# Kernel tuning notes

Hardware: AMD Instinct MI355X
Metric: run time of the kernel (lower is better)

## Reference

```python
import jax, jax.numpy as jnp
import numpy as np

DIM = 512
HEADS = 8
EPS = 1e-5


def layer_norm(x, g, b):
    mu = jnp.mean(x, axis=-1, keepdims=True)
    var = jnp.mean(jnp.square(x - mu), axis=-1, keepdims=True)
    return (x - mu) * jax.lax.rsqrt(var + EPS) * g + b


def setup_inputs() -> dict:
    key = jax.random.key(0)
    ks = jax.random.split(key, 8)
    d = DIM
    s = 0.02
    return {
        "x": jax.random.normal(ks[0], (2, d, 64, 64), jnp.float32),
        "ln1_g": jnp.ones((d,), jnp.float32),
        "ln1_b": jnp.zeros((d,), jnp.float32),
        "w_qkv": jax.random.normal(ks[1], (d, 3 * d), jnp.float32) * s,
        "b_qkv": jnp.zeros((3 * d,), jnp.float32),
        "w_proj": jax.random.normal(ks[2], (d, d), jnp.float32) * s,
        "b_proj": jnp.zeros((d,), jnp.float32),
        "ln2_g": jnp.ones((d,), jnp.float32),
        "ln2_b": jnp.zeros((d,), jnp.float32),
        "w_ffn1": jax.random.normal(ks[3], (d, 4 * d), jnp.float32) * s,
        "b_ffn1": jnp.zeros((4 * d,), jnp.float32),
        "w_ffn2": jax.random.normal(ks[4], (4 * d, d), jnp.float32) * s,
        "b_ffn2": jnp.zeros((d,), jnp.float32),
    }


def reference(x, ln1_g, ln1_b, w_qkv, b_qkv, w_proj, b_proj,
              ln2_g, ln2_b, w_ffn1, b_ffn1, w_ffn2, b_ffn2):
    B, C, H, W = x.shape
    hd = C // HEADS
    x_in = x
    t = x.reshape(B, C, H * W).transpose(0, 2, 1)  # [B, N, C]
    h = layer_norm(t, ln1_g, ln1_b)
    qkv = h @ w_qkv + b_qkv  # [B, N, 3C]
    q, k, v = jnp.split(qkv, 3, axis=-1)
    def to_heads(a):
        return a.reshape(B, -1, HEADS, hd).transpose(0, 2, 1, 3)  # [B, h, N, hd]
    q, k, v = to_heads(q), to_heads(k), to_heads(v)
    # NOTE: module scales by 1/sqrt(C), not 1/sqrt(head_dim)
    attn = jnp.einsum('bhqd,bhkd->bhqk', q, k) / jnp.sqrt(jnp.float32(C))
    attn = jax.nn.softmax(attn, axis=-1)
    out = jnp.einsum('bhqk,bhkd->bhqd', attn, v)
    out = out.transpose(0, 2, 1, 3).reshape(B, -1, C)
    out = out @ w_proj + b_proj
    t = t + out
    h2 = layer_norm(t, ln2_g, ln2_b)
    ffn = jax.nn.relu(h2 @ w_ffn1 + b_ffn1) @ w_ffn2 + b_ffn2
    t = t + ffn
    y = t.transpose(0, 2, 1).reshape(B, C, H, W)
    return y + x_in
```

## Files before the change

### kernel.cpp

```cpp
#include <hip/hip_runtime.h>
#include <hip/hip_bf16.h>

typedef __bf16 bf16;
typedef __bf16 bf16x8 __attribute__((ext_vector_type(8)));
typedef __bf16 bf16x4 __attribute__((ext_vector_type(4)));
typedef float f32x4 __attribute__((ext_vector_type(4)));
typedef int int4v __attribute__((ext_vector_type(4)));
typedef int int2v __attribute__((ext_vector_type(2)));

#define DEV static __device__ __forceinline__

DEV void gload16(const void* g, void* l) {
    __builtin_amdgcn_global_load_lds(
        (const __attribute__((address_space(1))) void*)g,
        (__attribute__((address_space(3))) void*)l, 16, 0, 0);
}

DEV f32x4 mfma16(bf16x8 a, bf16x8 b, f32x4 c) {
    return __builtin_amdgcn_mfma_f32_16x16x32_bf16(a, b, c, 0, 0, 0);
}

DEV int cvtpk(float lo, float hi) {
    int r;
    asm("v_cvt_pk_bf16_f32 %0, %1, %2" : "=v"(r) : "v"(lo), "v"(hi));
    return r;
}

DEV float rexp2(float x) {
    float r;
    asm("v_exp_f32 %0, %1" : "=v"(r) : "v"(x));
    return r;
}

__global__ __launch_bounds__(256)
void k_transpose_x(const float* __restrict__ x, float* __restrict__ t) {
    __shared__ float tile[32][33];
    int bid = blockIdx.x;
    int nt = bid & 127, ct = (bid >> 7) & 15, b = bid >> 11;
    int n0 = nt * 32, c0 = ct * 32;
    int tid = threadIdx.x;
    const float* xb = x + (size_t)b * 512 * 4096;
    int nl = tid & 31, cl = tid >> 5;
#pragma unroll
    for (int i = 0; i < 4; i++) {
        int c = cl + i * 8;
        tile[c][nl] = xb[(size_t)(c0 + c) * 4096 + n0 + nl];
    }
    __syncthreads();
    float* tb = t + (size_t)b * 4096 * 512;
    int cl2 = tid & 31, nl2 = tid >> 5;
#pragma unroll
    for (int i = 0; i < 4; i++) {
        int n = nl2 + i * 8;
        tb[(size_t)(n0 + n) * 512 + c0 + cl2] = tile[cl2][n];
    }
}

__global__ __launch_bounds__(256)
void k_out3(const float* __restrict__ t, const bf16* __restrict__ f2o,
            const float* __restrict__ x, float* __restrict__ y) {
    __shared__ float tile[32][33];
    int bid = blockIdx.x;
    int nt = bid & 127, ct = (bid >> 7) & 15, b = bid >> 11;
    int n0 = nt * 32, c0 = ct * 32;
    int tid = threadIdx.x;
#pragma unroll
    for (int i = 0; i < 4; i++) {
        int nl = (tid >> 5) + i * 8;
        size_t idx = (size_t)(b * 4096 + n0 + nl) * 512 + c0 + (tid & 31);
        tile[tid & 31][nl] = t[idx] + (float)f2o[idx];
    }
    __syncthreads();
    const float* xb = x + ((size_t)b * 512 + c0) * 4096;
    float* yb = y + ((size_t)b * 512 + c0) * 4096;
#pragma unroll
    for (int i = 0; i < 4; i++) {
        int cl = (tid >> 5) + i * 8;
        int nl = tid & 31;
        size_t off = (size_t)cl * 4096 + n0 + nl;
        yb[off] = tile[cl][nl] + xb[off];
    }
}

__global__ __launch_bounds__(256)
void k_ln(const float* __restrict__ t, const float* __restrict__ gg,
          const float* __restrict__ bb, bf16* __restrict__ h) {
    int lane = threadIdx.x & 63;
    int row = blockIdx.x * 4 + (threadIdx.x >> 6);
    const float* tr = t + (size_t)row * 512;
    f32x4 v0 = *(const f32x4*)(tr + lane * 4);
    f32x4 v1 = *(const f32x4*)(tr + 256 + lane * 4);
    float s = v0[0] + v0[1] + v0[2] + v0[3] + v1[0] + v1[1] + v1[2] + v1[3];
#pragma unroll
    for (int m = 1; m < 64; m <<= 1) s += __shfl_xor(s, m);
    float mu = s * (1.0f / 512.0f);
    float vs = 0.f;
#pragma unroll
    for (int j = 0; j < 4; j++) {
        float d0 = v0[j] - mu, d1 = v1[j] - mu;
        vs += d0 * d0 + d1 * d1;
    }
#pragma unroll
    for (int m = 1; m < 64; m <<= 1) vs += __shfl_xor(vs, m);
    float rs = rsqrtf(vs * (1.0f / 512.0f) + 1e-5f);
    f32x4 g0 = *(const f32x4*)(gg + lane * 4);
    f32x4 g1 = *(const f32x4*)(gg + 256 + lane * 4);
    f32x4 b0 = *(const f32x4*)(bb + lane * 4);
    f32x4 b1 = *(const f32x4*)(bb + 256 + lane * 4);
    bf16x4 o0, o1;
#pragma unroll
    for (int j = 0; j < 4; j++) {
        o0[j] = (bf16)((v0[j] - mu) * rs * g0[j] + b0[j]);
        o1[j] = (bf16)((v1[j] - mu) * rs * g1[j] + b1[j]);
    }
    *(bf16x4*)(h + (size_t)row * 512 + lane * 4) = o0;
    *(bf16x4*)(h + (size_t)row * 512 + 256 + lane * 4) = o1;
}

__global__ __launch_bounds__(256)
void k_lnr(float* __restrict__ t, const bf16* __restrict__ r,
           const float* __restrict__ gg, const float* __restrict__ bb,
           bf16* __restrict__ h) {
    int lane = threadIdx.x & 63;
    int row = blockIdx.x * 4 + (threadIdx.x >> 6);
    float* tr = t + (size_t)row * 512;
    f32x4 v0 = *(const f32x4*)(tr + lane * 4);
    f32x4 v1 = *(const f32x4*)(tr + 256 + lane * 4);
    bf16x4 r0 = *(const bf16x4*)(r + (size_t)row * 512 + lane * 4);
    bf16x4 r1 = *(const bf16x4*)(r + (size_t)row * 512 + 256 + lane * 4);
#pragma unroll
    for (int j = 0; j < 4; j++) {
        v0[j] += (float)r0[j];
        v1[j] += (float)r1[j];
    }
    *(f32x4*)(tr + lane * 4) = v0;
    *(f32x4*)(tr + 256 + lane * 4) = v1;
    float s = v0[0] + v0[1] + v0[2] + v0[3] + v1[0] + v1[1] + v1[2] + v1[3];
#pragma unroll
    for (int m = 1; m < 64; m <<= 1) s += __shfl_xor(s, m);
    float mu = s * (1.0f / 512.0f);
    float vs = 0.f;
#pragma unroll
    for (int j = 0; j < 4; j++) {
        float d0 = v0[j] - mu, d1 = v1[j] - mu;
        vs += d0 * d0 + d1 * d1;
    }
#pragma unroll
    for (int m = 1; m < 64; m <<= 1) vs += __shfl_xor(vs, m);
    float rs = rsqrtf(vs * (1.0f / 512.0f) + 1e-5f);
    f32x4 g0 = *(const f32x4*)(gg + lane * 4);
    f32x4 g1 = *(const f32x4*)(gg + 256 + lane * 4);
    f32x4 b0 = *(const f32x4*)(bb + lane * 4);
    f32x4 b1 = *(const f32x4*)(bb + 256 + lane * 4);
    bf16x4 o0, o1;
#pragma unroll
    for (int j = 0; j < 4; j++) {
        o0[j] = (bf16)((v0[j] - mu) * rs * g0[j] + b0[j]);
        o1[j] = (bf16)((v1[j] - mu) * rs * g1[j] + b1[j]);
    }
    *(bf16x4*)(h + (size_t)row * 512 + lane * 4) = o0;
    *(bf16x4*)(h + (size_t)row * 512 + 256 + lane * 4) = o1;
}

__global__ __launch_bounds__(256)
void k_wt(const float* __restrict__ w, bf16* __restrict__ wt, int K, int N) {
    __shared__ float tile[32][33];
    int ntn = N >> 5;
    int kt = blockIdx.x / ntn, ntile = blockIdx.x % ntn;
    int k0 = kt * 32, n0 = ntile * 32;
    int tid = threadIdx.x;
    int nl = tid & 31, kl = tid >> 5;
#pragma unroll
    for (int i = 0; i < 4; i++) {
        int k = kl + i * 8;
        tile[k][nl] = w[(size_t)(k0 + k) * N + n0 + nl];
    }
    __syncthreads();
    int kl2 = tid & 31, nl2 = tid >> 5;
#pragma unroll
    for (int i = 0; i < 4; i++) {
        int n = nl2 + i * 8;
        wt[(size_t)(n0 + n) * K + k0 + kl2] = (bf16)tile[kl2][n];
    }
}

template <int MODE>
__global__ __launch_bounds__(256, 2)
void k_gemm(const bf16* __restrict__ A, const bf16* __restrict__ BT,
            const float* __restrict__ bias, bf16* __restrict__ outb,
            bf16* __restrict__ vtout, int M, int N, int K) {
    __shared__ char smem[65536];
    int ntn = N >> 7;
    int nwg = gridDim.x;
    int bid = blockIdx.x;
    int cpx = nwg >> 3;
    bid = (bid & 7) * cpx + (bid >> 3);
    int bm = bid / ntn, bn = bid % ntn;
    int m0 = bm * 128, n0 = bn * 128;
    int tid = threadIdx.x;
    int w = tid >> 6, l = tid & 63;
    int wm = w >> 1, wn = w & 1;
    int l15 = l & 15, lg = l >> 4;

    f32x4 acc[4][4];
#pragma unroll
    for (int i = 0; i < 4; i++)
#pragma unroll
        for (int j = 0; j < 4; j++) acc[i][j] = (f32x4){0.f, 0.f, 0.f, 0.f};

    int srow = tid >> 3, sphys = tid & 7;
    int lrow_a = wm * 64 + l15;
    int lrow_b = wn * 64 + l15;

#define GEMM_STAGE(k0v, bb)                                                  \
    do {                                                                     \
        _Pragma("unroll") for (int s = 0; s < 4; s++) {                      \
            int row = s * 32 + srow;                                         \
            int k16 = sphys ^ (row & 7);                                     \
            gload16(A + (size_t)(m0 + row) * K + (k0v) + k16 * 8,            \
                    smem + (bb) * 16384 + s * 4096 + tid * 16);              \
            gload16(BT + (size_t)(n0 + row) * K + (k0v) + k16 * 8,           \
                    smem + 32768 + (bb) * 16384 + s * 4096 + tid * 16);      \
        }                                                                    \
    } while (0)

    int nk = K >> 6;
    GEMM_STAGE(0, 0);
    int cur = 0;
    for (int kt = 0; kt < nk; kt++) {
        if (kt + 1 < nk) {
            GEMM_STAGE((kt + 1) << 6, cur ^ 1);
            asm volatile("s_waitcnt vmcnt(8)" ::: "memory");
        } else {
            asm volatile("s_waitcnt vmcnt(0)" ::: "memory");
        }
        __builtin_amdgcn_s_barrier();
        __builtin_amdgcn_sched_barrier(0);
        const char* pA = smem + cur * 16384;
        const char* pB = smem + 32768 + cur * 16384;
#pragma unroll
        for (int ks = 0; ks < 2; ks++) {
            bf16x8 af[4], bfr[4];
#pragma unroll
            for (int rg = 0; rg < 4; rg++) {
                int row = lrow_a + rg * 16;
                af[rg] = *(const bf16x8*)(pA + row * 128 +
                                          (((lg + ks * 4) ^ (row & 7)) << 4));
            }
#pragma unroll
            for (int cg = 0; cg < 4; cg++) {
                int row = lrow_b + cg * 16;
                bfr[cg] = *(const bf16x8*)(pB + row * 128 +
                                           (((lg + ks * 4) ^ (row & 7)) << 4));
            }
#pragma unroll
            for (int rg = 0; rg < 4; rg++)
#pragma unroll
                for (int cg = 0; cg < 4; cg++)
                    acc[rg][cg] = mfma16(af[rg], bfr[cg], acc[rg][cg]);
        }
        __builtin_amdgcn_s_barrier();
        cur ^= 1;
    }
#undef GEMM_STAGE

    if (MODE == 2 && n0 >= 1024) {
        char* vl = smem;
#pragma unroll
        for (int cg = 0; cg < 4; cg++) {
            int col = wn * 64 + cg * 16 + l15;
            float bz = bias[n0 + col];
#pragma unroll
            for (int rg = 0; rg < 4; rg++) {
                int rowb = wm * 64 + rg * 16 + lg * 4;
                int2v qq = {cvtpk(acc[rg][cg][0] + bz, acc[rg][cg][1] + bz),
                            cvtpk(acc[rg][cg][2] + bz, acc[rg][cg][3] + bz)};
                *(int2v*)(vl + col * 272 + rowb * 2) = qq;
            }
        }
        __syncthreads();
        int b = m0 >> 12, nrow0 = m0 & 4095;
        int dl = tid >> 3, c8 = tid & 7;
#pragma unroll
        for (int dd = 0; dd < 4; dd++) {
            int d = dd * 32 + dl;
            int ch = (n0 - 1024) + d;
            bf16* dst = vtout +
                ((size_t)((b * 8 + (ch >> 6)) * 64 + (ch & 63))) * 4096 + nrow0;
#pragma unroll
            for (int half = 0; half < 2; half++) {
                int chunk = half * 8 + c8;
                bf16x8 vv = *(const bf16x8*)(vl + d * 272 + chunk * 16);
                *(bf16x8*)(dst + chunk * 8) = vv;
            }
        }
        return;
    }

    char* ep = smem;
#pragma unroll
    for (int cg = 0; cg < 4; cg++) {
        int lcol = wn * 64 + cg * 16 + l15;
        float bz = bias[n0 + lcol];
#pragma unroll
        for (int rg = 0; rg < 4; rg++) {
#pragma unroll
            for (int j = 0; j < 4; j++) {
                int lrow = wm * 64 + rg * 16 + lg * 4 + j;
                float v = acc[rg][cg][j] + bz;
                if (MODE == 1) v = fmaxf(v, 0.f);
                *(bf16*)(ep + lrow * 264 + lcol * 2) = (bf16)v;
            }
        }
    }
    __syncthreads();
    int cch = tid & 15, rof = tid >> 4;
#pragma unroll
    for (int i = 0; i < 8; i++) {
        int row = i * 16 + rof;
        bf16x8 vv = *(const bf16x8*)(ep + row * 264 + cch * 16);
        *(bf16x8*)(outb + (size_t)(m0 + row) * N + n0 + cch * 8) = vv;
    }
}

__global__ __launch_bounds__(256, 4)
void k_attn(const bf16* __restrict__ qkvb, const bf16* __restrict__ vt,
            bf16* __restrict__ attno) {
    __shared__ bf16 sK[2][64 * 64];
    __shared__ bf16 sV[2][64 * 64];
    const float sc = 0.044194173824159216f * 1.4426950408889634f;
    int bid = blockIdx.x;
    int nb = (bid & 7) * 128 + (bid >> 3);
    int bh = nb >> 6, qt = nb & 63;
    int b = bh >> 3, hh = bh & 7;
    int q0 = qt * 64;
    int tid = threadIdx.x, w = tid >> 6, l = tid & 63;
    int l15 = l & 15, lg = l >> 4, l7 = l15 & 7;
    int lg4 = lg * 4;
    int vperm = ((lg & 1) << 1) | (lg >> 1);
    const bf16* qbase = qkvb + (size_t)b * 4096 * 1536 + hh * 64;
    const bf16* kbase = qbase + 512;
    const bf16* vbase = vt + (size_t)bh * 64 * 4096;
    int srow = tid >> 3, sphys = tid & 7;

    const char* kp0 = (const char*)&sK[0][0] + l15 * 128 + ((lg ^ l7) << 4);
    const char* kp1 = (const char*)&sK[0][0] + l15 * 128 + (((4 + lg) ^ l7) << 4);
    const char* vp0 = (const char*)&sV[0][0] + l15 * 128 + ((vperm ^ l7) << 4);
    const char* vp1 = (const char*)&sV[0][0] + l15 * 128 + (((4 + vperm) ^ l7) << 4);
    char* dK0 = (char*)&sK[0][0] + tid * 16;
    char* dV0 = (char*)&sV[0][0] + tid * 16;
    const char* kg = (const char*)(kbase + srow * 1536 + (sphys ^ (srow & 7)) * 8);
    const char* vg = (const char*)(vbase + srow * 4096 + (sphys ^ (srow & 7)) * 8);

    gload16(kg, dK0);
    gload16(kg + 98304, dK0 + 4096);
    gload16(vg, dV0);
    gload16(vg + 262144, dV0 + 4096);
    kg += 196608;
    vg += 128;

    bf16x8 qf[2];
#pragma unroll
    for (int ks = 0; ks < 2; ks++) {
        bf16x8 v = *(const bf16x8*)(qbase +
            (size_t)(q0 + w * 16 + l15) * 1536 + ks * 32 + lg * 8);
        bf16x8 o;
#pragma unroll
        for (int j = 0; j < 8; j++) o[j] = (bf16)((float)v[j] * sc);
        qf[ks] = o;
    }

    float lsum = 0.f;
    f32x4 acc[4];
#pragma unroll
    for (int df = 0; df < 4; df++) acc[df] = (f32x4){0.f, 0.f, 0.f, 0.f};

#define ABODY(BUF, PF)                                                        \
    {                                                                         \
        if (PF) {                                                             \
            gload16(kg, dK0 + (1 - (BUF)) * 8192);                            \
            gload16(kg + 98304, dK0 + (1 - (BUF)) * 8192 + 4096);             \
            gload16(vg, dV0 + (1 - (BUF)) * 8192);                            \
            gload16(vg + 262144, dV0 + (1 - (BUF)) * 8192 + 4096);            \
            kg += 196608;                                                     \
            vg += 128;                                                        \
            asm volatile("s_waitcnt vmcnt(4)" ::: "memory");                  \
        } else {                                                              \
            asm volatile("s_waitcnt vmcnt(0)" ::: "memory");                  \
        }                                                                     \
        __builtin_amdgcn_s_barrier();                                         \
        __builtin_amdgcn_sched_barrier(0);                                    \
        f32x4 s0 = {0.f, 0.f, 0.f, 0.f}, s1 = s0, s2 = s0, s3 = s0;           \
        __builtin_amdgcn_s_setprio(1);                                        \
        s0 = mfma16(*(const bf16x8*)(kp0 + (BUF) * 8192 + 0 * 2048), qf[0], s0); \
        s1 = mfma16(*(const bf16x8*)(kp0 + (BUF) * 8192 + 1 * 2048), qf[0], s1); \
        s2 = mfma16(*(const bf16x8*)(kp0 + (BUF) * 8192 + 2 * 2048), qf[0], s2); \
        s3 = mfma16(*(const bf16x8*)(kp0 + (BUF) * 8192 + 3 * 2048), qf[0], s3); \
        s0 = mfma16(*(const bf16x8*)(kp1 + (BUF) * 8192 + 0 * 2048), qf[1], s0); \
        s1 = mfma16(*(const bf16x8*)(kp1 + (BUF) * 8192 + 1 * 2048), qf[1], s1); \
        s2 = mfma16(*(const bf16x8*)(kp1 + (BUF) * 8192 + 2 * 2048), qf[1], s2); \
        s3 = mfma16(*(const bf16x8*)(kp1 + (BUF) * 8192 + 3 * 2048), qf[1], s3); \
        __builtin_amdgcn_s_setprio(0);                                        \
        float e0 = rexp2(s0[0]), e1 = rexp2(s0[1]);                           \
        float e2 = rexp2(s0[2]), e3 = rexp2(s0[3]);                           \
        float e4 = rexp2(s1[0]), e5 = rexp2(s1[1]);                           \
        float e6 = rexp2(s1[2]), e7 = rexp2(s1[3]);                           \
        float e8 = rexp2(s2[0]), e9 = rexp2(s2[1]);                           \
        float e10 = rexp2(s2[2]), e11 = rexp2(s2[3]);                         \
        float e12 = rexp2(s3[0]), e13 = rexp2(s3[1]);                         \
        float e14 = rexp2(s3[2]), e15 = rexp2(s3[3]);                         \
        lsum += (((e0 + e1) + (e2 + e3)) + ((e4 + e5) + (e6 + e7))) +         \
                (((e8 + e9) + (e10 + e11)) + ((e12 + e13) + (e14 + e15)));    \
        int p0 = cvtpk(e0, e1), p1 = cvtpk(e2, e3);                           \
        int p2 = cvtpk(e4, e5), p3 = cvtpk(e6, e7);                           \
        int p4 = cvtpk(e8, e9), p5 = cvtpk(e10, e11);                         \
        int p6 = cvtpk(e12, e13), p7 = cvtpk(e14, e15);                       \
        asm("v_permlane16_swap_b32 %0, %1" : "+v"(p2), "+v"(p0));             \
        asm("v_permlane16_swap_b32 %0, %1" : "+v"(p3), "+v"(p1));             \
        asm("v_permlane16_swap_b32 %0, %1" : "+v"(p6), "+v"(p4));             \
        asm("v_permlane16_swap_b32 %0, %1" : "+v"(p7), "+v"(p5));             \
        {                                                                     \
            int4v ai = {p0, p1, p2, p3};                                      \
            bf16x8 af = __builtin_bit_cast(bf16x8, ai);                       \
            __builtin_amdgcn_s_setprio(1);                                    \
            acc[0] = mfma16(af, *(const bf16x8*)(vp0 + (BUF) * 8192 + 0 * 2048), acc[0]); \
            acc[1] = mfma16(af, *(const bf16x8*)(vp0 + (BUF) * 8192 + 1 * 2048), acc[1]); \
            acc[2] = mfma16(af, *(const bf16x8*)(vp0 + (BUF) * 8192 + 2 * 2048), acc[2]); \
            acc[3] = mfma16(af, *(const bf16x8*)(vp0 + (BUF) * 8192 + 3 * 2048), acc[3]); \
        }                                                                     \
        {                                                                     \
            int4v ai = {p4, p5, p6, p7};                                      \
            bf16x8 af = __builtin_bit_cast(bf16x8, ai);                       \
            acc[0] = mfma16(af, *(const bf16x8*)(vp1 + (BUF) * 8192 + 0 * 2048), acc[0]); \
            acc[1] = mfma16(af, *(const bf16x8*)(vp1 + (BUF) * 8192 + 1 * 2048), acc[1]); \
            acc[2] = mfma16(af, *(const bf16x8*)(vp1 + (BUF) * 8192 + 2 * 2048), acc[2]); \
            acc[3] = mfma16(af, *(const bf16x8*)(vp1 + (BUF) * 8192 + 3 * 2048), acc[3]); \
            __builtin_amdgcn_s_setprio(0);                                    \
        }                                                                     \
        __builtin_amdgcn_s_barrier();                                         \
    }

    for (int tt = 0; tt < 31; tt++) {
        ABODY(0, 1)
        ABODY(1, 1)
    }
    ABODY(0, 1)
    ABODY(1, 0)
#undef ABODY

    lsum += __shfl_xor(lsum, 16);
    lsum += __shfl_xor(lsum, 32);
    float invq[4];
#pragma unroll
    for (int j = 0; j < 4; j++)
        invq[j] = 1.0f / __shfl(lsum, lg4 + j);

    bf16* ow = (bf16*)&sK[0][0] + w * 16 * 64;
#pragma unroll
    for (int df = 0; df < 4; df++) {
        int chunk = df * 2 + (l15 >> 3);
        int within = l15 & 7;
#pragma unroll
        for (int j = 0; j < 4; j++) {
            int q = lg * 4 + j;
            *(bf16*)((char*)ow + q * 128 + ((chunk ^ (q & 7)) << 4) + within * 2) =
                (bf16)(acc[df][j] * invq[j]);
        }
    }
    __syncthreads();
    const char* owr = (const char*)ow;
#pragma unroll
    for (int half = 0; half < 2; half++) {
        int r = l >> 2, ch = (l & 3) + half * 4;
        bf16x8 vv = *(const bf16x8*)(owr + r * 128 + ((ch ^ (r & 7)) << 4));
        *(bf16x8*)(attno + (size_t)(b * 4096 + q0 + w * 16 + r) * 512 +
                   hh * 64 + ch * 8) = vv;
    }
}

extern "C" void kernel_launch(void* const* d_in, const int* in_sizes, int n_in,
                              void* d_out, int out_size, void* d_ws, size_t ws_size,
                              hipStream_t stream) {
    const float* x = (const float*)d_in[0];
    const float* ln1g = (const float*)d_in[1];
    const float* ln1b = (const float*)d_in[2];
    const float* wqkv = (const float*)d_in[3];
    const float* bqkv = (const float*)d_in[4];
    const float* wproj = (const float*)d_in[5];
    const float* bproj = (const float*)d_in[6];
    const float* ln2g = (const float*)d_in[7];
    const float* ln2b = (const float*)d_in[8];
    const float* wffn1 = (const float*)d_in[9];
    const float* bffn1 = (const float*)d_in[10];
    const float* wffn2 = (const float*)d_in[11];
    const float* bffn2 = (const float*)d_in[12];
    float* y = (float*)d_out;

    char* ws = (char*)d_ws;
    float* t    = (float*)(ws + 0);
    bf16* h     = (bf16*)(ws + 16777216);
    bf16* qkvb  = (bf16*)(ws + 25165824);
    bf16* vtb   = (bf16*)(ws + 50331648);
    bf16* f1    = (bf16*)(ws + 25165824);
    bf16* wqT   = (bf16*)(ws + 58720256);
    bf16* wpT   = (bf16*)(ws + 60293120);
    bf16* w1T   = (bf16*)(ws + 60817408);
    bf16* w2T   = (bf16*)(ws + 62914560);
    bf16* attno = h;
    bf16* po    = vtb;
    bf16* f2o   = h;

    k_transpose_x<<<4096, 256, 0, stream>>>(x, t);
    k_ln<<<2048, 256, 0, stream>>>(t, ln1g, ln1b, h);
    k_wt<<<(512 / 32) * (1536 / 32), 256, 0, stream>>>(wqkv, wqT, 512, 1536);
    k_wt<<<(512 / 32) * (512 / 32), 256, 0, stream>>>(wproj, wpT, 512, 512);
    k_wt<<<(512 / 32) * (2048 / 32), 256, 0, stream>>>(wffn1, w1T, 512, 2048);
    k_wt<<<(2048 / 32) * (512 / 32), 256, 0, stream>>>(wffn2, w2T, 2048, 512);

    k_gemm<2><<<768, 256, 0, stream>>>(h, wqT, bqkv, qkvb, vtb, 8192, 1536, 512);
    k_attn<<<1024, 256, 0, stream>>>(qkvb, vtb, attno);
    k_gemm<0><<<256, 256, 0, stream>>>(attno, wpT, bproj, po, nullptr, 8192, 512, 512);
    k_lnr<<<2048, 256, 0, stream>>>(t, po, ln2g, ln2b, h);
    k_gemm<1><<<1024, 256, 0, stream>>>(h, w1T, bffn1, f1, nullptr, 8192, 2048, 512);
    k_gemm<0><<<256, 256, 0, stream>>>(f1, w2T, bffn2, f2o, nullptr, 8192, 512, 2048);
    k_out3<<<4096, 256, 0, stream>>>(t, f2o, x, y);
}
```

Baseline: 203.7 us.

## Use 128x64 GEMM tiles for N=512 GEMMs and split attention softmax around MFMAs

New measurement: 201.2 us. About the same (-1.2%).

```diff
diff --git a/kernel.cpp b/kernel.cpp
--- a/kernel.cpp
+++ b/kernel.cpp
@@ -184,33 +184,35 @@
     }
 }
 
-template <int MODE>
-__global__ __launch_bounds__(256, 2)
+template <int MODE, int BN>
+__global__ __launch_bounds__(256, BN == 64 ? 3 : 2)
 void k_gemm(const bf16* __restrict__ A, const bf16* __restrict__ BT,
             const float* __restrict__ bias, bf16* __restrict__ outb,
             bf16* __restrict__ vtout, int M, int N, int K) {
-    __shared__ char smem[65536];
-    int ntn = N >> 7;
+    constexpr int CG = BN / 32;
+    constexpr int BSZ = CG * 4096;
+    __shared__ char smem[32768 + 2 * BSZ];
+    int ntn = N / BN;
     int nwg = gridDim.x;
     int bid = blockIdx.x;
     int cpx = nwg >> 3;
     bid = (bid & 7) * cpx + (bid >> 3);
     int bm = bid / ntn, bn = bid % ntn;
-    int m0 = bm * 128, n0 = bn * 128;
+    int m0 = bm * 128, n0 = bn * BN;
     int tid = threadIdx.x;
     int w = tid >> 6, l = tid & 63;
     int wm = w >> 1, wn = w & 1;
     int l15 = l & 15, lg = l >> 4;
 
-    f32x4 acc[4][4];
+    f32x4 acc[4][CG];
 #pragma unroll
     for (int i = 0; i < 4; i++)
 #pragma unroll
-        for (int j = 0; j < 4; j++) acc[i][j] = (f32x4){0.f, 0.f, 0.f, 0.f};
+        for (int j = 0; j < CG; j++) acc[i][j] = (f32x4){0.f, 0.f, 0.f, 0.f};
 
     int srow = tid >> 3, sphys = tid & 7;
     int lrow_a = wm * 64 + l15;
-    int lrow_b = wn * 64 + l15;
+    int lrow_b = wn * (BN / 2) + l15;
 
 #define GEMM_STAGE(k0v, bb)                                                  \
     do {                                                                     \
@@ -219,8 +221,12 @@
             int k16 = sphys ^ (row & 7);                                     \
             gload16(A + (size_t)(m0 + row) * K + (k0v) + k16 * 8,            \
                     smem + (bb) * 16384 + s * 4096 + tid * 16);              \
+        }                                                                    \
+        _Pragma("unroll") for (int s = 0; s < CG; s++) {                     \
+            int row = s * 32 + srow;                                         \
+            int k16 = sphys ^ (row & 7);                                     \
             gload16(BT + (size_t)(n0 + row) * K + (k0v) + k16 * 8,           \
-                    smem + 32768 + (bb) * 16384 + s * 4096 + tid * 16);      \
+                    smem + 32768 + (bb) * BSZ + s * 4096 + tid * 16);        \
         }                                                                    \
     } while (0)
 
@@ -230,17 +236,20 @@
     for (int kt = 0; kt < nk; kt++) {
         if (kt + 1 < nk) {
             GEMM_STAGE((kt + 1) << 6, cur ^ 1);
-            asm volatile("s_waitcnt vmcnt(8)" ::: "memory");
+            if constexpr (BN == 128)
+                asm volatile("s_waitcnt vmcnt(8)" ::: "memory");
+            else
+                asm volatile("s_waitcnt vmcnt(6)" ::: "memory");
         } else {
             asm volatile("s_waitcnt vmcnt(0)" ::: "memory");
         }
         __builtin_amdgcn_s_barrier();
         __builtin_amdgcn_sched_barrier(0);
         const char* pA = smem + cur * 16384;
-        const char* pB = smem + 32768 + cur * 16384;
+        const char* pB = smem + 32768 + cur * BSZ;
 #pragma unroll
         for (int ks = 0; ks < 2; ks++) {
-            bf16x8 af[4], bfr[4];
+            bf16x8 af[4], bfr[CG];
 #pragma unroll
             for (int rg = 0; rg < 4; rg++) {
                 int row = lrow_a + rg * 16;
@@ -248,7 +257,7 @@
                                           (((lg + ks * 4) ^ (row & 7)) << 4));
             }
 #pragma unroll
-            for (int cg = 0; cg < 4; cg++) {
+            for (int cg = 0; cg < CG; cg++) {
                 int row = lrow_b + cg * 16;
                 bfr[cg] = *(const bf16x8*)(pB + row * 128 +
                                            (((lg + ks * 4) ^ (row & 7)) << 4));
@@ -256,7 +265,7 @@
 #pragma unroll
             for (int rg = 0; rg < 4; rg++)
 #pragma unroll
-                for (int cg = 0; cg < 4; cg++)
+                for (int cg = 0; cg < CG; cg++)
                     acc[rg][cg] = mfma16(af[rg], bfr[cg], acc[rg][cg]);
         }
         __builtin_amdgcn_s_barrier();
@@ -264,43 +273,47 @@
     }
 #undef GEMM_STAGE
 
-    if (MODE == 2 && n0 >= 1024) {
-        char* vl = smem;
-#pragma unroll
-        for (int cg = 0; cg < 4; cg++) {
-            int col = wn * 64 + cg * 16 + l15;
-            float bz = bias[n0 + col];
-#pragma unroll
-            for (int rg = 0; rg < 4; rg++) {
-                int rowb = wm * 64 + rg * 16 + lg * 4;
-                int2v qq = {cvtpk(acc[rg][cg][0] + bz, acc[rg][cg][1] + bz),
-                            cvtpk(acc[rg][cg][2] + bz, acc[rg][cg][3] + bz)};
-                *(int2v*)(vl + col * 272 + rowb * 2) = qq;
+    if constexpr (MODE == 2) {
+        if (n0 >= 1024) {
+            char* vl = smem;
+#pragma unroll
+            for (int cg = 0; cg < CG; cg++) {
+                int col = wn * 64 + cg * 16 + l15;
+                float bz = bias[n0 + col];
+#pragma unroll
+                for (int rg = 0; rg < 4; rg++) {
+                    int rowb = wm * 64 + rg * 16 + lg * 4;
+                    int2v qq = {cvtpk(acc[rg][cg][0] + bz, acc[rg][cg][1] + bz),
+                                cvtpk(acc[rg][cg][2] + bz, acc[rg][cg][3] + bz)};
+                    *(int2v*)(vl + col * 272 + rowb * 2) = qq;
+                }
             }
+            __syncthreads();
+            int b = m0 >> 12, nrow0 = m0 & 4095;
+            int dl = tid >> 3, c8 = tid & 7;
+#pragma unroll
+            for (int dd = 0; dd < 4; dd++) {
+                int d = dd * 32 + dl;
+                int ch = (n0 - 1024) + d;
+                bf16* dst = vtout +
+                    ((size_t)((b * 8 + (ch >> 6)) * 64 + (ch & 63))) * 4096 + nrow0;
+#pragma unroll
+                for (int half = 0; half < 2; half++) {
+                    int chunk = half * 8 + c8;
+                    bf16x8 vv = *(const bf16x8*)(vl + d * 272 + chunk * 16);
+                    *(bf16x8*)(dst + chunk * 8) = vv;
+                }
+            }
+            return;
         }
-        __syncthreads();
-        int b = m0 >> 12, nrow0 = m0 & 4095;
-        int dl = tid >> 3, c8 = tid & 7;
-#pragma unroll
-        for (int dd = 0; dd < 4; dd++) {
-            int d = dd * 32 + dl;
-            int ch = (n0 - 1024) + d;
-            bf16* dst = vtout +
-                ((size_t)((b * 8 + (ch >> 6)) * 64 + (ch & 63))) * 4096 + nrow0;
-#pragma unroll
-            for (int half = 0; half < 2; half++) {
-                int chunk = half * 8 + c8;
-                bf16x8 vv = *(const bf16x8*)(vl + d * 272 + chunk * 16);
-                *(bf16x8*)(dst + chunk * 8) = vv;
-            }
-        }
-        return;
-    }
-
+    }
+
+    constexpr int RS = BN * 2 + 8;
+    constexpr int CH = BN / 8;
     char* ep = smem;
 #pragma unroll
-    for (int cg = 0; cg < 4; cg++) {
-        int lcol = wn * 64 + cg * 16 + l15;
+    for (int cg = 0; cg < CG; cg++) {
+        int lcol = wn * (BN / 2) + cg * 16 + l15;
         float bz = bias[n0 + lcol];
 #pragma unroll
         for (int rg = 0; rg < 4; rg++) {
@@ -309,16 +322,18 @@
                 int lrow = wm * 64 + rg * 16 + lg * 4 + j;
                 float v = acc[rg][cg][j] + bz;
                 if (MODE == 1) v = fmaxf(v, 0.f);
-                *(bf16*)(ep + lrow * 264 + lcol * 2) = (bf16)v;
+                *(bf16*)(ep + lrow * RS + lcol * 2) = (bf16)v;
             }
         }
     }
     __syncthreads();
-    int cch = tid & 15, rof = tid >> 4;
-#pragma unroll
-    for (int i = 0; i < 8; i++) {
-        int row = i * 16 + rof;
-        bf16x8 vv = *(const bf16x8*)(ep + row * 264 + cch * 16);
+    int cch = tid & (CH - 1);
+    int rof = tid / CH;
+    constexpr int RPP = 256 / CH;
+#pragma unroll
+    for (int i = 0; i < 128 / RPP; i++) {
+        int row = i * RPP + rof;
+        bf16x8 vv = *(const bf16x8*)(ep + row * RS + cch * 16);
         *(bf16x8*)(outb + (size_t)(m0 + row) * N + n0 + cch * 8) = vv;
     }
 }
@@ -370,10 +385,11 @@
         qf[ks] = o;
     }
 
+    const f32x4 kZ = {0.f, 0.f, 0.f, 0.f};
     float lsum = 0.f;
     f32x4 acc[4];
 #pragma unroll
-    for (int df = 0; df < 4; df++) acc[df] = (f32x4){0.f, 0.f, 0.f, 0.f};
+    for (int df = 0; df < 4; df++) acc[df] = kZ;
 
 #define ABODY(BUF, PF)                                                        \
     {                                                                         \
@@ -390,35 +406,27 @@
         }                                                                     \
         __builtin_amdgcn_s_barrier();                                         \
         __builtin_amdgcn_sched_barrier(0);                                    \
-        f32x4 s0 = {0.f, 0.f, 0.f, 0.f}, s1 = s0, s2 = s0, s3 = s0;           \
+        f32x4 s0, s1, s2, s3;                                                 \
         __builtin_amdgcn_s_setprio(1);                                        \
-        s0 = mfma16(*(const bf16x8*)(kp0 + (BUF) * 8192 + 0 * 2048), qf[0], s0); \
-        s1 = mfma16(*(const bf16x8*)(kp0 + (BUF) * 8192 + 1 * 2048), qf[0], s1); \
-        s2 = mfma16(*(const bf16x8*)(kp0 + (BUF) * 8192 + 2 * 2048), qf[0], s2); \
-        s3 = mfma16(*(const bf16x8*)(kp0 + (BUF) * 8192 + 3 * 2048), qf[0], s3); \
+        s0 = mfma16(*(const bf16x8*)(kp0 + (BUF) * 8192 + 0 * 2048), qf[0], kZ); \
         s0 = mfma16(*(const bf16x8*)(kp1 + (BUF) * 8192 + 0 * 2048), qf[1], s0); \
+        s1 = mfma16(*(const bf16x8*)(kp0 + (BUF) * 8192 + 1 * 2048), qf[0], kZ); \
         s1 = mfma16(*(const bf16x8*)(kp1 + (BUF) * 8192 + 1 * 2048), qf[1], s1); \
-        s2 = mfma16(*(const bf16x8*)(kp1 + (BUF) * 8192 + 2 * 2048), qf[1], s2); \
-        s3 = mfma16(*(const bf16x8*)(kp1 + (BUF) * 8192 + 3 * 2048), qf[1], s3); \
         __builtin_amdgcn_s_setprio(0);                                        \
         float e0 = rexp2(s0[0]), e1 = rexp2(s0[1]);                           \
         float e2 = rexp2(s0[2]), e3 = rexp2(s0[3]);                           \
         float e4 = rexp2(s1[0]), e5 = rexp2(s1[1]);                           \
         float e6 = rexp2(s1[2]), e7 = rexp2(s1[3]);                           \
-        float e8 = rexp2(s2[0]), e9 = rexp2(s2[1]);                           \
-        float e10 = rexp2(s2[2]), e11 = rexp2(s2[3]);                         \
-        float e12 = rexp2(s3[0]), e13 = rexp2(s3[1]);                         \
-        float e14 = rexp2(s3[2]), e15 = rexp2(s3[3]);                         \
-        lsum += (((e0 + e1) + (e2 + e3)) + ((e4 + e5) + (e6 + e7))) +         \
-                (((e8 + e9) + (e10 + e11)) + ((e12 + e13) + (e14 + e15)));    \
+        __builtin_amdgcn_s_setprio(1);                                        \
+        s2 = mfma16(*(const bf16x8*)(kp0 + (BUF) * 8192 + 2 * 2048), qf[0], kZ); \
+        s2 = mfma16(*(const bf16x8*)(kp1 + (BUF) * 8192 + 2 * 2048), qf[1], s2); \
+        s3 = mfma16(*(const bf16x8*)(kp0 + (BUF) * 8192 + 3 * 2048), qf[0], kZ); \
+        s3 = mfma16(*(const bf16x8*)(kp1 + (BUF) * 8192 + 3 * 2048), qf[1], s3); \
+        __builtin_amdgcn_s_setprio(0);                                        \
         int p0 = cvtpk(e0, e1), p1 = cvtpk(e2, e3);                           \
         int p2 = cvtpk(e4, e5), p3 = cvtpk(e6, e7);                           \
-        int p4 = cvtpk(e8, e9), p5 = cvtpk(e10, e11);                         \
-        int p6 = cvtpk(e12, e13), p7 = cvtpk(e14, e15);                       \
         asm("v_permlane16_swap_b32 %0, %1" : "+v"(p2), "+v"(p0));             \
         asm("v_permlane16_swap_b32 %0, %1" : "+v"(p3), "+v"(p1));             \
-        asm("v_permlane16_swap_b32 %0, %1" : "+v"(p6), "+v"(p4));             \
-        asm("v_permlane16_swap_b32 %0, %1" : "+v"(p7), "+v"(p5));             \
         {                                                                     \
             int4v ai = {p0, p1, p2, p3};                                      \
             bf16x8 af = __builtin_bit_cast(bf16x8, ai);                       \
@@ -427,16 +435,28 @@
             acc[1] = mfma16(af, *(const bf16x8*)(vp0 + (BUF) * 8192 + 1 * 2048), acc[1]); \
             acc[2] = mfma16(af, *(const bf16x8*)(vp0 + (BUF) * 8192 + 2 * 2048), acc[2]); \
             acc[3] = mfma16(af, *(const bf16x8*)(vp0 + (BUF) * 8192 + 3 * 2048), acc[3]); \
+            __builtin_amdgcn_s_setprio(0);                                    \
         }                                                                     \
+        float e8 = rexp2(s2[0]), e9 = rexp2(s2[1]);                           \
+        float e10 = rexp2(s2[2]), e11 = rexp2(s2[3]);                         \
+        float e12 = rexp2(s3[0]), e13 = rexp2(s3[1]);                         \
+        float e14 = rexp2(s3[2]), e15 = rexp2(s3[3]);                         \
+        int p4 = cvtpk(e8, e9), p5 = cvtpk(e10, e11);                         \
+        int p6 = cvtpk(e12, e13), p7 = cvtpk(e14, e15);                       \
+        asm("v_permlane16_swap_b32 %0, %1" : "+v"(p6), "+v"(p4));             \
+        asm("v_permlane16_swap_b32 %0, %1" : "+v"(p7), "+v"(p5));             \
         {                                                                     \
             int4v ai = {p4, p5, p6, p7};                                      \
             bf16x8 af = __builtin_bit_cast(bf16x8, ai);                       \
+            __builtin_amdgcn_s_setprio(1);                                    \
             acc[0] = mfma16(af, *(const bf16x8*)(vp1 + (BUF) * 8192 + 0 * 2048), acc[0]); \
             acc[1] = mfma16(af, *(const bf16x8*)(vp1 + (BUF) * 8192 + 1 * 2048), acc[1]); \
             acc[2] = mfma16(af, *(const bf16x8*)(vp1 + (BUF) * 8192 + 2 * 2048), acc[2]); \
             acc[3] = mfma16(af, *(const bf16x8*)(vp1 + (BUF) * 8192 + 3 * 2048), acc[3]); \
             __builtin_amdgcn_s_setprio(0);                                    \
         }                                                                     \
+        lsum += (((e0 + e1) + (e2 + e3)) + ((e4 + e5) + (e6 + e7))) +         \
+                (((e8 + e9) + (e10 + e11)) + ((e12 + e13) + (e14 + e15)));    \
         __builtin_amdgcn_s_barrier();                                         \
     }
 
@@ -517,11 +537,11 @@
     k_wt<<<(512 / 32) * (2048 / 32), 256, 0, stream>>>(wffn1, w1T, 512, 2048);
     k_wt<<<(2048 / 32) * (512 / 32), 256, 0, stream>>>(wffn2, w2T, 2048, 512);
 
-    k_gemm<2><<<768, 256, 0, stream>>>(h, wqT, bqkv, qkvb, vtb, 8192, 1536, 512);
+    k_gemm<2, 128><<<768, 256, 0, stream>>>(h, wqT, bqkv, qkvb, vtb, 8192, 1536, 512);
     k_attn<<<1024, 256, 0, stream>>>(qkvb, vtb, attno);
-    k_gemm<0><<<256, 256, 0, stream>>>(attno, wpT, bproj, po, nullptr, 8192, 512, 512);
+    k_gemm<0, 64><<<512, 256, 0, stream>>>(attno, wpT, bproj, po, nullptr, 8192, 512, 512);
     k_lnr<<<2048, 256, 0, stream>>>(t, po, ln2g, ln2b, h);
-    k_gemm<1><<<1024, 256, 0, stream>>>(h, w1T, bffn1, f1, nullptr, 8192, 2048, 512);
-    k_gemm<0><<<256, 256, 0, stream>>>(f1, w2T, bffn2, f2o, nullptr, 8192, 512, 2048);
+    k_gemm<1, 128><<<1024, 256, 0, stream>>>(h, w1T, bffn1, f1, nullptr, 8192, 2048, 512);
+    k_gemm<0, 64><<<512, 256, 0, stream>>>(f1, w2T, bffn2, f2o, nullptr, 8192, 512, 2048);
     k_out3<<<4096, 256, 0, stream>>>(t, f2o, x, y);
 }
```
